# Kernel optimization log

Hardware: AMD Instinct MI355X
Metric: run time of the kernel (lower is better)

Reference implementation:

```python
import jax, jax.numpy as jnp
import numpy as np

N = 10000      # nodes
E = 320000     # edges (avg degree 32)
D_IN = 128
D_H = 256
D_C = 32       # comm_dim
D_OUT = 64


def setup_inputs() -> dict:
    key = jax.random.key(0)
    ks = jax.random.split(key, 14)
    p = lambda k, shape: jax.random.normal(k, shape, jnp.float32) * 0.02
    return {
        "x": jax.random.normal(ks[0], (N, D_IN), jnp.float32),
        "edge_index": jax.random.randint(ks[1], (2, E), 0, N),
        "W_in": p(ks[2], (D_IN, D_H)), "b_in": jnp.zeros((D_H,), jnp.float32),
        "Wq": p(ks[3], (D_H, D_C)),   "bq": jnp.zeros((D_C,), jnp.float32),
        "Wk": p(ks[4], (D_H, D_C)),   "bk": jnp.zeros((D_C,), jnp.float32),
        "Wv": p(ks[5], (D_H, D_H)),   "bv": jnp.zeros((D_H,), jnp.float32),
        "W1": p(ks[6], (2 * D_H, D_H)), "b1": jnp.zeros((D_H,), jnp.float32),
        "W2": p(ks[7], (D_H, D_OUT)),  "b2": jnp.zeros((D_OUT,), jnp.float32),
    }


def reference(x, edge_index, W_in, b_in, Wq, bq, Wk, bk, Wv, bv, W1, b1, W2, b2):
    n = x.shape[0]
    h = x @ W_in + b_in                       # [N, D_H]
    q = h @ Wq + bq                           # [N, D_C]
    k = h @ Wk + bk                           # [N, D_C]
    v = h @ Wv + bv                           # [N, D_H]
    scores = (q @ k.T) / np.sqrt(q.shape[-1]).astype(np.float32)  # [N, N]
    # torch: zeros -> scatter 1 at edges -> masked_fill(==0, -inf);
    # edge positions keep value 1.0 ADDED to scores (faithful quirk).
    mask = jnp.full((n, n), -jnp.inf, jnp.float32)
    mask = mask.at[edge_index[0], edge_index[1]].set(1.0)
    w = jax.nn.softmax(scores + mask, axis=-1)
    w = jnp.nan_to_num(w, nan=0.0)            # rows with no edges -> all zeros
    comm = w @ v                              # [N, D_H]
    combined = jnp.concatenate([h, comm], axis=-1)  # [N, 2*D_H]
    return jax.nn.relu(combined @ W1 + b1) @ W2 + b2  # [N, D_OUT]
```

## Files before the change

kernel.cpp:

```cpp
#include <hip/hip_runtime.h>
#include <stdint.h>
#include <stddef.h>

constexpr int N_NODES = 10000;
constexpr int N_EDGES = 320000;
constexpr int DIM_IN  = 128;
constexpr int DIM_H   = 256;
constexpr int DIM_C   = 32;
constexpr int DIM_OUT = 64;
constexpr int DIM_QKV = DIM_C + DIM_C + DIM_H;
constexpr int DIM_QK  = 2 * DIM_C;
constexpr int DIM_CAT = 2 * DIM_H;
constexpr float SCALE = 0.17677669529663687f;
constexpr int MAXD = 192;
constexpr float VSCALE = 64.0f;
constexpr int PAD  = 40;
constexpr int PAD2 = 72;
constexpr int HP   = 264;

#if __has_builtin(__builtin_amdgcn_cvt_pk_f32_fp8) && __has_builtin(__builtin_amdgcn_cvt_pk_fp8_f32)
#define V_FP8 1
#else
#define V_FP8 0
#endif

constexpr size_t alignw(size_t w) { return (w + 15) & ~size_t(15); }
constexpr size_t OFF_DEG   = 0;
constexpr size_t OFF_COL   = alignw(OFF_DEG + N_NODES);
constexpr size_t OFF_QK    = alignw(OFF_COL + (size_t)N_NODES * MAXD);
constexpr size_t OFF_VT    = alignw(OFF_QK + (size_t)N_NODES * DIM_QK);
constexpr size_t OFF_CATBF = alignw(OFF_VT + (size_t)N_NODES * DIM_H / 2);
constexpr size_t OFF_WINT  = alignw(OFF_CATBF + (size_t)N_NODES * DIM_CAT / 2);
constexpr size_t OFF_WQKVT = alignw(OFF_WINT + (size_t)DIM_H * DIM_IN / 2);
constexpr size_t OFF_W1T   = alignw(OFF_WQKVT + (size_t)DIM_QKV * DIM_H / 2);
constexpr size_t OFF_W2T   = alignw(OFF_W1T + (size_t)DIM_H * DIM_CAT / 2);

typedef __attribute__((ext_vector_type(8))) short short8;
typedef __attribute__((ext_vector_type(4))) float floatx4;
typedef __attribute__((ext_vector_type(2))) float floatx2;

#define MFMA16 __builtin_amdgcn_mfma_f32_16x16x32_bf16

__device__ inline unsigned short f2bf(float f) {
    uint32_t u = __builtin_bit_cast(uint32_t, f);
    uint32_t r = (u + 0x7fffu + ((u >> 16) & 1u)) >> 16;
    return (unsigned short)r;
}
__device__ inline float bf2f_lo(uint32_t u) { return __builtin_bit_cast(float, u << 16); }
__device__ inline float bf2f_hi(uint32_t u) { return __builtin_bit_cast(float, u & 0xffff0000u); }

__global__ void prep_w(const float* __restrict__ W_in,
                       const float* __restrict__ Wq, const float* __restrict__ Wk,
                       const float* __restrict__ Wv,
                       int* __restrict__ deg,
                       unsigned short* __restrict__ WinT, unsigned short* __restrict__ WqkvT)
{
    const int i0 = blockIdx.x * blockDim.x + threadIdx.x;
    const int stride = gridDim.x * blockDim.x;
    for (int i = i0; i < N_NODES; i += stride) deg[i] = 0;
    for (int idx = i0; idx < DIM_IN * DIM_H; idx += stride) {
        int k = idx >> 8, n = idx & 255;
        WinT[n * DIM_IN + k] = f2bf(W_in[idx]);
    }
    for (int idx = i0; idx < DIM_H * DIM_C; idx += stride) {
        int k = idx >> 5, n = idx & 31;
        WqkvT[n * DIM_H + k] = f2bf(Wq[idx]);
    }
    for (int idx = i0; idx < DIM_H * DIM_C; idx += stride) {
        int k = idx >> 5, n = idx & 31;
        WqkvT[(DIM_C + n) * DIM_H + k] = f2bf(Wk[idx]);
    }
    for (int idx = i0; idx < DIM_H * DIM_H; idx += stride) {
        int k = idx >> 8, n = idx & 255;
        WqkvT[(2 * DIM_C + n) * DIM_H + k] = f2bf(Wv[idx]);
    }
}

__global__ __launch_bounds__(256)
void gemm12(const float* __restrict__ x, const int* __restrict__ ei,
            const unsigned short* __restrict__ WinT, const float* __restrict__ b_in,
            const unsigned short* __restrict__ WqkvT,
            const float* __restrict__ bq, const float* __restrict__ bk,
            const float* __restrict__ bv,
            const float* __restrict__ W1, const float* __restrict__ W2,
            int* __restrict__ deg, int* __restrict__ col,
            unsigned short* __restrict__ cat_bf, float* __restrict__ qk,
            unsigned short* __restrict__ v_tab,
            unsigned short* __restrict__ W1T, unsigned short* __restrict__ W2T)
{
    __shared__ alignas(16) char SMEM[62976];
    short* hS  = (short*)SMEM;
    short* As1 = (short*)(SMEM + 16896);
    short* Bs1 = (short*)(SMEM + 21504);
    short* Bs2 = (short*)(SMEM + 16896);
    const int tid   = threadIdx.x;
    const int bid   = blockIdx.x;
    const int wave  = tid >> 6;
    const int lane  = tid & 63;
    const int quad  = lane >> 4;
    const int col16 = lane & 15;
    const int sr    = tid >> 3;
    const int sc    = (tid & 7) * 8;
    const int row0  = bid * 32;

    {
        const int stride = gridDim.x * 256;
        const int i0 = bid * 256 + tid;
        int s4[4], d4[4]; bool ok[4];
        #pragma unroll
        for (int t = 0; t < 4; ++t) {
            int e = i0 + t * stride;
            ok[t] = e < N_EDGES;
            s4[t] = ok[t] ? ei[e] : 0;
            d4[t] = ok[t] ? ei[N_EDGES + e] : 0;
        }
        #pragma unroll
        for (int t = 0; t < 4; ++t)
            if (ok[t]) {
                int slot = atomicAdd(&deg[s4[t]], 1);
                if (slot < MAXD) col[s4[t] * MAXD + slot] = d4[t];
            }
    }

    floatx4 acc[2][4] = {};
    for (int k0 = 0; k0 < DIM_IN; k0 += 64) {
        {
            int gr = row0 + sr;
            float4 a = {}, b = {};
            if (gr < N_NODES) {
                const float4* xp = (const float4*)(x + (size_t)gr * DIM_IN + k0 + sc);
                a = xp[0]; b = xp[1];
            }
            uint4 o;
            o.x = (uint32_t)f2bf(a.x) | ((uint32_t)f2bf(a.y) << 16);
            o.y = (uint32_t)f2bf(a.z) | ((uint32_t)f2bf(a.w) << 16);
            o.z = (uint32_t)f2bf(b.x) | ((uint32_t)f2bf(b.y) << 16);
            o.w = (uint32_t)f2bf(b.z) | ((uint32_t)f2bf(b.w) << 16);
            *(uint4*)(As1 + sr * PAD2 + sc) = o;
        }
        #pragma unroll
        for (int p = 0; p < 8; ++p) {
            int r = sr + p * 32;
            *(short8*)(Bs1 + r * PAD2 + sc) =
                *(const short8*)(WinT + (size_t)r * DIM_IN + k0 + sc);
        }
        __syncthreads();
        short8 af[2][2], bfr[4][2];
        #pragma unroll
        for (int m = 0; m < 2; ++m)
            #pragma unroll
            for (int kh = 0; kh < 2; ++kh)
                af[m][kh] = *(const short8*)(As1 + (m * 16 + col16) * PAD2 + kh * 32 + quad * 8);
        #pragma unroll
        for (int n = 0; n < 4; ++n)
            #pragma unroll
            for (int kh = 0; kh < 2; ++kh)
                bfr[n][kh] = *(const short8*)(Bs1 + (wave * 64 + n * 16 + col16) * PAD2 + kh * 32 + quad * 8);
        #pragma unroll
        for (int m = 0; m < 2; ++m)
            #pragma unroll
            for (int n = 0; n < 4; ++n)
                #pragma unroll
                for (int kh = 0; kh < 2; ++kh)
                    acc[m][n] = MFMA16(af[m][kh], bfr[n][kh], acc[m][n], 0, 0, 0);
        __syncthreads();
    }
    #pragma unroll
    for (int m = 0; m < 2; ++m)
        #pragma unroll
        for (int n = 0; n < 4; ++n) {
            int gc = wave * 64 + n * 16 + col16;
            float bia = b_in[gc];
            #pragma unroll
            for (int r = 0; r < 4; ++r) {
                int lr = m * 16 + quad * 4 + r;
                unsigned short hv = f2bf(acc[m][n][r] + bia);
                hS[lr * HP + gc] = (short)hv;
                if (row0 + lr < N_NODES) cat_bf[(size_t)(row0 + lr) * DIM_CAT + gc] = hv;
            }
        }
    __syncthreads();

    floatx4 acc2[2][5] = {};
    for (int k0 = 0; k0 < DIM_H; k0 += 64) {
        #pragma unroll
        for (int p = 0; p < 10; ++p) {
            int r = sr + p * 32;
            *(short8*)(Bs2 + r * PAD2 + sc) =
                *(const short8*)(WqkvT + (size_t)r * DIM_H + k0 + sc);
        }
        __syncthreads();
        short8 af[2][2], bfr[5][2];
        #pragma unroll
        for (int m = 0; m < 2; ++m)
            #pragma unroll
            for (int kh = 0; kh < 2; ++kh)
                af[m][kh] = *(const short8*)(hS + (m * 16 + col16) * HP + k0 + kh * 32 + quad * 8);
        #pragma unroll
        for (int n = 0; n < 5; ++n)
            #pragma unroll
            for (int kh = 0; kh < 2; ++kh)
                bfr[n][kh] = *(const short8*)(Bs2 + (wave * 80 + n * 16 + col16) * PAD2 + kh * 32 + quad * 8);
        #pragma unroll
        for (int m = 0; m < 2; ++m)
            #pragma unroll
            for (int n = 0; n < 5; ++n)
                #pragma unroll
                for (int kh = 0; kh < 2; ++kh)
                    acc2[m][n] = MFMA16(af[m][kh], bfr[n][kh], acc2[m][n], 0, 0, 0);
        __syncthreads();
    }
    #pragma unroll
    for (int m = 0; m < 2; ++m)
        #pragma unroll
        for (int n = 0; n < 5; ++n) {
            int gc = wave * 80 + n * 16 + col16;
            float bia = (gc < DIM_C) ? bq[gc] : (gc < DIM_QK) ? bk[gc - DIM_C] : bv[gc - DIM_QK];
            #pragma unroll
            for (int r = 0; r < 4; ++r) {
                int gr = row0 + m * 16 + quad * 4 + r;
                if (gr >= N_NODES) continue;
                float v = acc2[m][n][r] + bia;
                if (gc < DIM_QK) {
                    qk[(size_t)gr * DIM_QK + gc] = v;
                } else {
#if V_FP8
                    int pk = __builtin_amdgcn_cvt_pk_fp8_f32(v * VSCALE, 0.f, 0, false);
                    ((unsigned char*)v_tab)[(size_t)gr * DIM_H + (gc - DIM_QK)] =
                        (unsigned char)(pk & 0xff);
#else
                    v_tab[(size_t)gr * DIM_H + (gc - DIM_QK)] = f2bf(v);
#endif
                }
            }
        }

    {
        const int stride = gridDim.x * 256;
        const int i0 = bid * 256 + tid;
        for (int idx = i0; idx < DIM_CAT * DIM_H; idx += stride) {
            int k = idx >> 8, n = idx & 255;
            W1T[n * DIM_CAT + k] = f2bf(W1[idx]);
        }
        for (int idx = i0; idx < DIM_H * DIM_OUT; idx += stride) {
            int k = idx >> 6, n = idx & 63;
            W2T[n * DIM_H + k] = f2bf(W2[idx]);
        }
    }
}

__global__ __launch_bounds__(256)
void attn_row(const float* __restrict__ qk, const unsigned short* __restrict__ v_tab,
              const int* __restrict__ deg, const int* __restrict__ col,
              unsigned short* __restrict__ cat_bf) {
    __shared__ int   dstS[4][MAXD];
    __shared__ float wS[4][MAXD];
    __shared__ float qS[4][DIM_C];
    const int wave = threadIdx.x >> 6;
    const int lane = threadIdx.x & 63;
    const int row = blockIdx.x * 4 + wave;
    int d = deg[row];
    if (d > MAXD) d = MAXD;
    const int* crow = col + (size_t)row * MAXD;

    for (int p = lane; p < d; p += 64) dstS[wave][p] = crow[p];
    if (lane < DIM_C) qS[wave][lane] = qk[(size_t)row * DIM_QK + lane];
    __syncthreads();

    float mysum = 0.f;
    if (d <= 64) {
        int mydst = (lane < d) ? dstS[wave][lane] : -1;
        bool dup = false;
        for (int k2 = 0; k2 < d - 1; ++k2) {
            int other = __shfl(mydst, k2, 64);
            dup = dup || (k2 < lane && other == mydst);
        }
        float w = 0.f;
        if (lane < d && !dup) {
            const float4* kp = (const float4*)(qk + (size_t)mydst * DIM_QK + DIM_C);
            float s = 0.f;
            #pragma unroll
            for (int i = 0; i < DIM_C / 4; ++i) {
                float4 b = kp[i];
                s += qS[wave][4 * i + 0] * b.x + qS[wave][4 * i + 1] * b.y
                   + qS[wave][4 * i + 2] * b.z + qS[wave][4 * i + 3] * b.w;
            }
            w = expf(s * SCALE);
        }
        wS[wave][lane] = w;
        mysum = w;
    } else {
        for (int p = lane; p < d; p += 64) {
            int mydst = dstS[wave][p];
            bool dup = false;
            for (int j = 0; j < p; ++j) dup = dup || (dstS[wave][j] == mydst);
            float w = 0.f;
            if (!dup) {
                const float4* kp = (const float4*)(qk + (size_t)mydst * DIM_QK + DIM_C);
                float s = 0.f;
                #pragma unroll
                for (int i = 0; i < DIM_C / 4; ++i) {
                    float4 b = kp[i];
                    s += qS[wave][4 * i + 0] * b.x + qS[wave][4 * i + 1] * b.y
                       + qS[wave][4 * i + 2] * b.z + qS[wave][4 * i + 3] * b.w;
                }
                w = expf(s * SCALE);
            }
            wS[wave][p] = w;
            mysum += w;
        }
    }
    #pragma unroll
    for (int off = 32; off; off >>= 1) mysum += __shfl_down(mysum, off, 64);
    float total = __shfl(mysum, 0, 64);
#if V_FP8
    float inv = (d > 0 && total > 0.f) ? 1.0f / (total * VSCALE) : 0.f;
#else
    float inv = (d > 0 && total > 0.f) ? 1.0f / total : 0.f;
#endif
    __syncthreads();

    float4 acc = make_float4(0.f, 0.f, 0.f, 0.f);
#if V_FP8
    const uint32_t* vb = (const uint32_t*)v_tab;
#else
    const uint2* vb = (const uint2*)v_tab;
#endif
    for (int p0 = 0; p0 < d; p0 += 16) {
        int j[16]; float w[16];
        #pragma unroll
        for (int t = 0; t < 16; ++t) {
            int idx = p0 + t;
            bool in = idx < d;
            j[t] = in ? dstS[wave][idx] : 0;
            w[t] = in ? wS[wave][idx] : 0.f;
        }
#if V_FP8
        uint32_t r[16];
        #pragma unroll
        for (int t = 0; t < 16; ++t) r[t] = vb[(size_t)j[t] * 64 + lane];
        #pragma unroll
        for (int t = 0; t < 16; ++t) {
            floatx2 lo = __builtin_amdgcn_cvt_pk_f32_fp8(r[t], false);
            floatx2 hi = __builtin_amdgcn_cvt_pk_f32_fp8(r[t], true);
            acc.x += w[t] * lo.x; acc.y += w[t] * lo.y;
            acc.z += w[t] * hi.x; acc.w += w[t] * hi.y;
        }
#else
        uint2 r[16];
        #pragma unroll
        for (int t = 0; t < 16; ++t) r[t] = vb[(size_t)j[t] * 64 + lane];
        #pragma unroll
        for (int t = 0; t < 16; ++t) {
            acc.x += w[t] * bf2f_lo(r[t].x);
            acc.y += w[t] * bf2f_hi(r[t].x);
            acc.z += w[t] * bf2f_lo(r[t].y);
            acc.w += w[t] * bf2f_hi(r[t].y);
        }
#endif
    }
    acc.x *= inv; acc.y *= inv; acc.z *= inv; acc.w *= inv;
    uint2 o;
    o.x = (uint32_t)f2bf(acc.x) | ((uint32_t)f2bf(acc.y) << 16);
    o.y = (uint32_t)f2bf(acc.z) | ((uint32_t)f2bf(acc.w) << 16);
    *(uint2*)(cat_bf + (size_t)row * DIM_CAT + DIM_H + lane * 4) = o;
}

__global__ __launch_bounds__(256)
void gemm_w1w2(const unsigned short* __restrict__ cat, const unsigned short* __restrict__ W1T,
               const float* __restrict__ b1, const unsigned short* __restrict__ W2T,
               const float* __restrict__ b2, float* __restrict__ out, int M)
{
    constexpr int TP = 260;
    __shared__ short As[32 * PAD2];
    __shared__ short BsTs[256 * PAD2];
    short* Bs = BsTs;
    short* Ts = BsTs;
    const int tid   = threadIdx.x;
    const int wave  = tid >> 6;
    const int lane  = tid & 63;
    const int quad  = lane >> 4;
    const int col16 = lane & 15;
    const int row0  = blockIdx.x * 32;

    const int sr = tid >> 3;
    const int sc = (tid & 7) * 8;

    floatx4 acc[2][4] = {};
    for (int k0 = 0; k0 < DIM_CAT; k0 += 64) {
        {
            int gr = row0 + sr;
            short8 v = {};
            if (gr < M) v = *(const short8*)(cat + (size_t)gr * DIM_CAT + k0 + sc);
            *(short8*)(As + sr * PAD2 + sc) = v;
        }
        #pragma unroll
        for (int p = 0; p < 8; ++p) {
            int r = sr + p * 32;
            *(short8*)(Bs + r * PAD2 + sc) = *(const short8*)(W1T + (size_t)r * DIM_CAT + k0 + sc);
        }
        __syncthreads();
        short8 af[2][2], bfr[4][2];
        #pragma unroll
        for (int m = 0; m < 2; ++m)
            #pragma unroll
            for (int kh = 0; kh < 2; ++kh)
                af[m][kh] = *(const short8*)(As + (m * 16 + col16) * PAD2 + kh * 32 + quad * 8);
        #pragma unroll
        for (int n = 0; n < 4; ++n)
            #pragma unroll
            for (int kh = 0; kh < 2; ++kh)
                bfr[n][kh] = *(const short8*)(Bs + (wave * 64 + n * 16 + col16) * PAD2 + kh * 32 + quad * 8);
        #pragma unroll
        for (int m = 0; m < 2; ++m)
            #pragma unroll
            for (int n = 0; n < 4; ++n)
                #pragma unroll
                for (int kh = 0; kh < 2; ++kh)
                    acc[m][n] = MFMA16(af[m][kh], bfr[n][kh], acc[m][n], 0, 0, 0);
        __syncthreads();
    }

    #pragma unroll
    for (int m = 0; m < 2; ++m)
        #pragma unroll
        for (int n = 0; n < 4; ++n) {
            int gc = wave * 64 + n * 16 + col16;
            float bia = b1[gc];
            #pragma unroll
            for (int r = 0; r < 4; ++r) {
                int lr = m * 16 + quad * 4 + r;
                Ts[lr * TP + gc] = (short)f2bf(fmaxf(acc[m][n][r] + bia, 0.f));
            }
        }
    __syncthreads();

    floatx4 acc2[2] = {};
    for (int k0 = 0; k0 < DIM_H; k0 += 32) {
        short8 b = *(const short8*)(W2T + (size_t)(wave * 16 + col16) * DIM_H + k0 + quad * 8);
        #pragma unroll
        for (int m = 0; m < 2; ++m) {
            short8 a = *(const short8*)(Ts + (m * 16 + col16) * TP + k0 + quad * 8);
            acc2[m] = MFMA16(a, b, acc2[m], 0, 0, 0);
        }
    }
    #pragma unroll
    for (int m = 0; m < 2; ++m) {
        int gc = wave * 16 + col16;
        float bia = b2[gc];
        #pragma unroll
        for (int r = 0; r < 4; ++r) {
            int gr = row0 + m * 16 + quad * 4 + r;
            if (gr < M) out[(size_t)gr * DIM_OUT + gc] = acc2[m][r] + bia;
        }
    }
}

extern "C" void kernel_launch(void* const* d_in, const int* in_sizes, int n_in,
                              void* d_out, int out_size, void* d_ws, size_t ws_size,
                              hipStream_t stream) {
    (void)in_sizes; (void)n_in; (void)out_size; (void)ws_size;
    const float* x    = (const float*)d_in[0];
    const int*   ei   = (const int*)d_in[1];
    const float* W_in = (const float*)d_in[2];
    const float* b_in = (const float*)d_in[3];
    const float* Wq   = (const float*)d_in[4];
    const float* bq   = (const float*)d_in[5];
    const float* Wk   = (const float*)d_in[6];
    const float* bk   = (const float*)d_in[7];
    const float* Wv   = (const float*)d_in[8];
    const float* bv   = (const float*)d_in[9];
    const float* W1   = (const float*)d_in[10];
    const float* b1   = (const float*)d_in[11];
    const float* W2   = (const float*)d_in[12];
    const float* b2   = (const float*)d_in[13];
    float* out = (float*)d_out;

    uint32_t* ws      = (uint32_t*)d_ws;
    int*      deg     = (int*)(ws + OFF_DEG);
    int*      col     = (int*)(ws + OFF_COL);
    float*    qk      = (float*)(ws + OFF_QK);
    unsigned short* v_tab  = (unsigned short*)(ws + OFF_VT);
    unsigned short* cat_bf = (unsigned short*)(ws + OFF_CATBF);
    unsigned short* WinT   = (unsigned short*)(ws + OFF_WINT);
    unsigned short* WqkvT  = (unsigned short*)(ws + OFF_WQKVT);
    unsigned short* W1T    = (unsigned short*)(ws + OFF_W1T);
    unsigned short* W2T    = (unsigned short*)(ws + OFF_W2T);

    prep_w<<<256, 256, 0, stream>>>(W_in, Wq, Wk, Wv, deg, WinT, WqkvT);
    gemm12<<<(N_NODES + 31) / 32, 256, 0, stream>>>(
        x, ei, WinT, b_in, WqkvT, bq, bk, bv, W1, W2,
        deg, col, cat_bf, qk, v_tab, W1T, W2T);
    attn_row<<<N_NODES / 4, 256, 0, stream>>>(qk, v_tab, deg, col, cat_bf);
    gemm_w1w2<<<(N_NODES + 31) / 32, 256, 0, stream>>>(
        cat_bf, W1T, b1, W2T, b2, out, N_NODES);
}
```

Measured before the change: 166.7 us.

## Register-prefetch GEMM tiles, move edge CSR build after GEMMs, vectorize dedup scan

```diff
diff --git a/kernel.cpp b/kernel.cpp
--- a/kernel.cpp
+++ b/kernel.cpp
@@ -14,11 +14,10 @@
 constexpr float SCALE = 0.17677669529663687f;
 constexpr int MAXD = 192;
 constexpr float VSCALE = 64.0f;
-constexpr int PAD  = 40;
 constexpr int PAD2 = 72;
 constexpr int HP   = 264;
 
-#if __has_builtin(__builtin_amdgcn_cvt_pk_f32_fp8) && __has_builtin(__builtin_amdgcn_cvt_pk_fp8_f32)
+#if __has_builtin(__builtin_amdgcn_cvt_pk_f32_fp8) && __has_builtin(__builtin_amdgcn_cvt_pk_f32_fp8)
 #define V_FP8 1
 #else
 #define V_FP8 0
@@ -102,47 +101,46 @@
     const int sr    = tid >> 3;
     const int sc    = (tid & 7) * 8;
     const int row0  = bid * 32;
-
-    {
-        const int stride = gridDim.x * 256;
-        const int i0 = bid * 256 + tid;
-        int s4[4], d4[4]; bool ok[4];
-        #pragma unroll
-        for (int t = 0; t < 4; ++t) {
-            int e = i0 + t * stride;
-            ok[t] = e < N_EDGES;
-            s4[t] = ok[t] ? ei[e] : 0;
-            d4[t] = ok[t] ? ei[N_EDGES + e] : 0;
-        }
-        #pragma unroll
-        for (int t = 0; t < 4; ++t)
-            if (ok[t]) {
-                int slot = atomicAdd(&deg[s4[t]], 1);
-                if (slot < MAXD) col[s4[t] * MAXD + slot] = d4[t];
-            }
-    }
-
+    const int gr_s  = row0 + sr;
+
+    float4 xa = {}, xb = {};
+    if (gr_s < N_NODES) {
+        const float4* xp = (const float4*)(x + (size_t)gr_s * DIM_IN + sc);
+        xa = xp[0]; xb = xp[1];
+    }
+    short8 wreg[8];
+    #pragma unroll
+    for (int p = 0; p < 8; ++p)
+        wreg[p] = *(const short8*)(WinT + (size_t)(sr + p * 32) * DIM_IN + sc);
+
+    short8 breg[10];
     floatx4 acc[2][4] = {};
+    #pragma unroll
     for (int k0 = 0; k0 < DIM_IN; k0 += 64) {
         {
-            int gr = row0 + sr;
-            float4 a = {}, b = {};
-            if (gr < N_NODES) {
-                const float4* xp = (const float4*)(x + (size_t)gr * DIM_IN + k0 + sc);
-                a = xp[0]; b = xp[1];
-            }
             uint4 o;
-            o.x = (uint32_t)f2bf(a.x) | ((uint32_t)f2bf(a.y) << 16);
-            o.y = (uint32_t)f2bf(a.z) | ((uint32_t)f2bf(a.w) << 16);
-            o.z = (uint32_t)f2bf(b.x) | ((uint32_t)f2bf(b.y) << 16);
-            o.w = (uint32_t)f2bf(b.z) | ((uint32_t)f2bf(b.w) << 16);
+            o.x = (uint32_t)f2bf(xa.x) | ((uint32_t)f2bf(xa.y) << 16);
+            o.y = (uint32_t)f2bf(xa.z) | ((uint32_t)f2bf(xa.w) << 16);
+            o.z = (uint32_t)f2bf(xb.x) | ((uint32_t)f2bf(xb.y) << 16);
+            o.w = (uint32_t)f2bf(xb.z) | ((uint32_t)f2bf(xb.w) << 16);
             *(uint4*)(As1 + sr * PAD2 + sc) = o;
         }
         #pragma unroll
-        for (int p = 0; p < 8; ++p) {
-            int r = sr + p * 32;
-            *(short8*)(Bs1 + r * PAD2 + sc) =
-                *(const short8*)(WinT + (size_t)r * DIM_IN + k0 + sc);
+        for (int p = 0; p < 8; ++p)
+            *(short8*)(Bs1 + (sr + p * 32) * PAD2 + sc) = wreg[p];
+        if (k0 + 64 < DIM_IN) {
+            xa = {}; xb = {};
+            if (gr_s < N_NODES) {
+                const float4* xp = (const float4*)(x + (size_t)gr_s * DIM_IN + (k0 + 64) + sc);
+                xa = xp[0]; xb = xp[1];
+            }
+            #pragma unroll
+            for (int p = 0; p < 8; ++p)
+                wreg[p] = *(const short8*)(WinT + (size_t)(sr + p * 32) * DIM_IN + (k0 + 64) + sc);
+        } else {
+            #pragma unroll
+            for (int p = 0; p < 10; ++p)
+                breg[p] = *(const short8*)(WqkvT + (size_t)(sr + p * 32) * DIM_H + sc);
         }
         __syncthreads();
         short8 af[2][2], bfr[4][2];
@@ -182,12 +180,15 @@
     __syncthreads();
 
     floatx4 acc2[2][5] = {};
+    #pragma unroll
     for (int k0 = 0; k0 < DIM_H; k0 += 64) {
         #pragma unroll
-        for (int p = 0; p < 10; ++p) {
-            int r = sr + p * 32;
-            *(short8*)(Bs2 + r * PAD2 + sc) =
-                *(const short8*)(WqkvT + (size_t)r * DIM_H + k0 + sc);
+        for (int p = 0; p < 10; ++p)
+            *(short8*)(Bs2 + (sr + p * 32) * PAD2 + sc) = breg[p];
+        if (k0 + 64 < DIM_H) {
+            #pragma unroll
+            for (int p = 0; p < 10; ++p)
+                breg[p] = *(const short8*)(WqkvT + (size_t)(sr + p * 32) * DIM_H + (k0 + 64) + sc);
         }
         __syncthreads();
         short8 af[2][2], bfr[5][2];
@@ -238,6 +239,20 @@
     {
         const int stride = gridDim.x * 256;
         const int i0 = bid * 256 + tid;
+        int s4[4], d4[4]; bool ok[4];
+        #pragma unroll
+        for (int t = 0; t < 4; ++t) {
+            int e = i0 + t * stride;
+            ok[t] = e < N_EDGES;
+            s4[t] = ok[t] ? ei[e] : 0;
+            d4[t] = ok[t] ? ei[N_EDGES + e] : 0;
+        }
+        #pragma unroll
+        for (int t = 0; t < 4; ++t)
+            if (ok[t]) {
+                int slot = atomicAdd(&deg[s4[t]], 1);
+                if (slot < MAXD) col[s4[t] * MAXD + slot] = d4[t];
+            }
         for (int idx = i0; idx < DIM_CAT * DIM_H; idx += stride) {
             int k = idx >> 8, n = idx & 255;
             W1T[n * DIM_CAT + k] = f2bf(W1[idx]);
@@ -253,7 +268,7 @@
 void attn_row(const float* __restrict__ qk, const unsigned short* __restrict__ v_tab,
               const int* __restrict__ deg, const int* __restrict__ col,
               unsigned short* __restrict__ cat_bf) {
-    __shared__ int   dstS[4][MAXD];
+    __shared__ alignas(16) int dstS[4][MAXD];
     __shared__ float wS[4][MAXD];
     __shared__ float qS[4][DIM_C];
     const int wave = threadIdx.x >> 6;
@@ -271,9 +286,16 @@
     if (d <= 64) {
         int mydst = (lane < d) ? dstS[wave][lane] : -1;
         bool dup = false;
-        for (int k2 = 0; k2 < d - 1; ++k2) {
-            int other = __shfl(mydst, k2, 64);
-            dup = dup || (k2 < lane && other == mydst);
+        {
+            const int4* ds4 = (const int4*)(&dstS[wave][0]);
+            const int lim = (lane < d) ? lane : 0;
+            for (int j0 = 0; j0 < lim; j0 += 4) {
+                int4 v = ds4[j0 >> 2];
+                dup = dup || (v.x == mydst)
+                   || (j0 + 1 < lim && v.y == mydst)
+                   || (j0 + 2 < lim && v.z == mydst)
+                   || (j0 + 3 < lim && v.w == mydst);
+            }
         }
         float w = 0.f;
         if (lane < d && !dup) {
@@ -385,19 +407,28 @@
 
     const int sr = tid >> 3;
     const int sc = (tid & 7) * 8;
+    const int gr_s = row0 + sr;
+
+    short8 areg = {};
+    if (gr_s < M) areg = *(const short8*)(cat + (size_t)gr_s * DIM_CAT + sc);
+    short8 breg[8];
+    #pragma unroll
+    for (int p = 0; p < 8; ++p)
+        breg[p] = *(const short8*)(W1T + (size_t)(sr + p * 32) * DIM_CAT + sc);
 
     floatx4 acc[2][4] = {};
+    #pragma unroll
     for (int k0 = 0; k0 < DIM_CAT; k0 += 64) {
-        {
-            int gr = row0 + sr;
-            short8 v = {};
-            if (gr < M) v = *(const short8*)(cat + (size_t)gr * DIM_CAT + k0 + sc);
-            *(short8*)(As + sr * PAD2 + sc) = v;
-        }
-        #pragma unroll
-        for (int p = 0; p < 8; ++p) {
-            int r = sr + p * 32;
-            *(short8*)(Bs + r * PAD2 + sc) = *(const short8*)(W1T + (size_t)r * DIM_CAT + k0 + sc);
+        *(short8*)(As + sr * PAD2 + sc) = areg;
+        #pragma unroll
+        for (int p = 0; p < 8; ++p)
+            *(short8*)(Bs + (sr + p * 32) * PAD2 + sc) = breg[p];
+        if (k0 + 64 < DIM_CAT) {
+            areg = short8{};
+            if (gr_s < M) areg = *(const short8*)(cat + (size_t)gr_s * DIM_CAT + (k0 + 64) + sc);
+            #pragma unroll
+            for (int p = 0; p < 8; ++p)
+                breg[p] = *(const short8*)(W1T + (size_t)(sr + p * 32) * DIM_CAT + (k0 + 64) + sc);
         }
         __syncthreads();
         short8 af[2][2], bfr[4][2];
@@ -436,6 +467,7 @@
     __syncthreads();
 
     floatx4 acc2[2] = {};
+    #pragma unroll
     for (int k0 = 0; k0 < DIM_H; k0 += 32) {
         short8 b = *(const short8*)(W2T + (size_t)(wave * 16 + col16) * DIM_H + k0 + quad * 8);
         #pragma unroll
```

Result: faster. 162.1 us (-2.7%).
